# Performance work log

Measured on AMD Instinct MI355X. Metric: run time of the kernel, lower is better.

Reference implementation:

```python
import jax, jax.numpy as jnp
import numpy as np

POOL_K = 8        # predictor_kernel_size
THRESH = 0.05     # predictor_threshold
EPS = 1e-5        # masked_fill value


def _round_ste(x):
    # straight-through round (forward: round)
    return x + jax.lax.stop_gradient(jnp.round(x) - x)


def _quant_act_uint(x, scale, bits):
    # Brevitas Uint8ActPerTensorFloat-style fake quant: unsigned, per-tensor scale
    n = 2.0 ** bits - 1.0
    return jnp.clip(_round_ste(x / scale), 0.0, n) * scale


def _quant_weight_per_oc(w, bits):
    # signed, narrow-range, per-output-channel scaling: s = max|w| / (2^(b-1)-1)
    n = 2.0 ** (bits - 1) - 1.0
    s = jnp.max(jnp.abs(w), axis=(1, 2, 3), keepdims=True) / n
    return jnp.clip(_round_ste(w / s), -n, n) * s


def _conv(x, w):
    return jax.lax.conv_general_dilated(
        x, w, window_strides=(1, 1), padding=((1, 1), (1, 1)),
        dimension_numbers=('NCHW', 'OIHW', 'NCHW'))


def _predictor_mask(x):
    # AvgPool2d(8) (stride=kernel) -> threshold -> nearest upsample back to HxW
    B, C, H, W = x.shape
    pooled = x.reshape(B, C, H // POOL_K, POOL_K, W // POOL_K, POOL_K).mean(axis=(3, 5))
    m = pooled >= THRESH
    m = jnp.repeat(jnp.repeat(m, POOL_K, axis=2), POOL_K, axis=3)  # nearest interp
    return jax.lax.stop_gradient(m)  # mask.detach()


def setup_inputs() -> dict:
    key = jax.random.key(0)
    k1, k2, k3 = jax.random.split(key, 3)
    x = jax.random.normal(k1, (32, 128, 56, 56), jnp.float32)
    w_high = jax.random.normal(k2, (128, 128, 3, 3), jnp.float32) * 0.05
    w_low = jax.random.normal(k3, (128, 128, 3, 3), jnp.float32) * 0.05
    return {
        'x': x,
        'w_high': w_high,
        'w_low': w_low,
        'act_scale_high': jnp.float32(0.02),
        'act_scale_low': jnp.float32(0.04),
    }


def reference(x, w_high, w_low, act_scale_high, act_scale_low):
    mask = _predictor_mask(x)                 # [B,C,H,W] bool
    x_high = jnp.where(mask, x, EPS)          # masked_fill(~mask, 1e-5)
    x_low = jnp.where(mask, EPS, x)           # masked_fill(mask, 1e-5)
    y_high = _conv(_quant_act_uint(x_high, act_scale_high, 8),
                   _quant_weight_per_oc(w_high, 8))
    y_low = _conv(_quant_act_uint(x_low, act_scale_low, 4),
                  _quant_weight_per_oc(w_low, 4))
    return y_high + y_low
```

## Files before the change

### kernel.cpp

```cpp
#include <hip/hip_runtime.h>
#include <hip/hip_bf16.h>
#include <stdint.h>

#define BATCH 32
#define CH 128
#define HH 56
#define WW 56
#define HW 3136
#define M_TOTAL (BATCH*HW)
#define PLANE ((size_t)M_TOTAL * 16)

using int4v   = __attribute__((ext_vector_type(4))) int;
using float4v = __attribute__((ext_vector_type(4))) float;

#define WQB_OFF 0
#define SCB_OFF 294912
#define ZP_OFF  296448
#define AQN_OFF 296704

#define GLD_LDS16(g, l)                                                        \
  __builtin_amdgcn_global_load_lds(                                            \
      (const __attribute__((address_space(1))) void*)(g),                      \
      (__attribute__((address_space(3))) void*)(l), 16, 0, 0)

#define KSTR 484

__global__ __launch_bounds__(256) void prep_kernel(
    const float* __restrict__ x,
    const float* __restrict__ wh, const float* __restrict__ wl,
    const float* __restrict__ p_sh, const float* __restrict__ p_sl,
    char* __restrict__ wqb, float* __restrict__ scb, int* __restrict__ zp,
    char* __restrict__ aqn) {
  __shared__ __align__(16) float smem[16 * KSTR + 128];
  int t = threadIdx.x;

  if (blockIdx.x >= BATCH * 7 * 8) {
    int blk = blockIdx.x - BATCH * 7 * 8;
    int which = blk >> 7, oc = blk & 127;
    if (blk == 0 && t < 64)
      zp[t] = (t < 32) ? 0x80808080 : 0;
    const float* src = (which ? wl : wh) + (size_t)oc * 1152;
    float n = which ? 7.0f : 127.0f;
    float* red = smem;
    int* ired = (int*)(smem + 256);

    float m = 0.0f;
    for (int e = t; e < 1152; e += 256) m = fmaxf(m, fabsf(src[e]));
    red[t] = m;
    __syncthreads();
    for (int s = 128; s > 0; s >>= 1) {
      if (t < s) red[t] = fmaxf(red[t], red[t + s]);
      __syncthreads();
    }
    float scale = red[0] / n;

    int partial = 0;
    for (int e = t; e < 1152; e += 256) {
      int tt = e >> 7, ic = e & 127;
      float q = rintf(src[ic * 9 + tt] / scale);
      q = fminf(fmaxf(q, -n), n);
      int k = (int)q;
      partial += k;
      wqb[((size_t)tt * 128 + oc) * 256 + which * 128 + ic] = (char)k;
    }
    ired[t] = partial;
    __syncthreads();
    for (int s = 128; s > 0; s >>= 1) {
      if (t < s) ired[t] += ired[t + s];
      __syncthreads();
    }
    if (t == 0) {
      float s_act = which ? p_sl[0] : p_sh[0];
      float sc = s_act * scale;
      if (which == 0) {
        scb[oc] = sc;
        scb[256 + oc] = sc * 128.0f * (float)ired[0];
      } else {
        scb[128 + oc] = sc;
      }
    }
    return;
  }

  int bi = blockIdx.x;
  int cg = bi & 7;
  int bb = bi >> 3;
  int b = bb / 7, band = bb - b * 7;
  float* sx = smem;
  float* smk = smem + 16 * KSTR;
  #pragma unroll
  for (int i = 0; i < 7; ++i) {
    int idx = i * 256 + t;
    int k = idx / 112, rem = idx - k * 112;
    int r = rem / 14, w4 = rem - r * 14;
    *(float4v*)(sx + k * KSTR + r * 60 + w4 * 4) =
        *(const float4v*)(x + ((size_t)(b * 128 + cg * 16 + k)) * HW
                            + (band * 8 + r) * 56 + w4 * 4);
  }
  __syncthreads();
  if (t < 112) {
    int k = t / 7, bw = t - (t / 7) * 7;
    float s = 0.0f;
    #pragma unroll
    for (int r = 0; r < 8; ++r)
      #pragma unroll
      for (int j = 0; j < 8; ++j)
        s += sx[k * KSTR + r * 60 + bw * 8 + j];
    smk[t] = (s * (1.0f / 64.0f) >= 0.05f) ? 1.0f : 0.0f;
  }
  __syncthreads();
  float shs = p_sh[0], sls = p_sl[0];
  #pragma unroll
  for (int it = 0; it < 2; ++it) {
    int pos = it * 256 + t;
    if (pos < 448) {
      int r = pos / 56, w = pos - r * 56;
      int h = band * 8 + r;
      size_t gp = (size_t)b * HW + (size_t)h * 56 + w;
      int hw_[4] = {0, 0, 0, 0}, lw_[4] = {0, 0, 0, 0};
      int mcell = w >> 3;
      #pragma unroll
      for (int k = 0; k < 16; ++k) {
        float xv = sx[k * KSTR + r * 60 + w];
        bool mk = smk[k * 7 + mcell] != 0.0f;
        float xh = mk ? xv : 1e-5f;
        int kh = (int)fminf(fmaxf(rintf(xh / shs), 0.0f), 255.0f) - 128;
        float xl = mk ? 1e-5f : xv;
        int kl = (int)fminf(fmaxf(rintf(xl / sls), 0.0f), 15.0f);
        hw_[k >> 2] |= (kh & 0xff) << ((k & 3) * 8);
        lw_[k >> 2] |= (kl & 0xff) << ((k & 3) * 8);
      }
      *(int4v*)(aqn + ((size_t)cg * M_TOTAL + gp) * 16) =
          (int4v){hw_[0], hw_[1], hw_[2], hw_[3]};
      *(int4v*)(aqn + ((size_t)(8 + cg) * M_TOTAL + gp) * 16) =
          (int4v){lw_[0], lw_[1], lw_[2], lw_[3]};
    }
  }
}

__global__ __launch_bounds__(512, 4) void conv_mfma_kernel(
    const char* __restrict__ wqb,
    const char* __restrict__ aqn,
    const char* __restrict__ zp,
    const float* __restrict__ scb,
    float* __restrict__ out) {
  __shared__ __align__(16) char As[2][160 * 64];
  __shared__ __align__(16) char Bs[2][384 * 64];

  int tid = threadIdx.x;
  int lane = tid & 63, wv = tid >> 6;
  int wm = wv >> 2, wn = wv & 3;
  int lr = lane & 15, quad = lane >> 4;
  int bx = blockIdx.x;
  int m0 = (((bx & 7) * 98) + (bx >> 3)) * 128;

  int ng = (wv < 2) ? 2 : 1;
  int sgrp[2] = {wv, wv + 8};
  const char* abase[2];
  const char* zbase[2];
  int avalid[2], ah[2];
  #pragma unroll
  for (int j = 0; j < 2; ++j) {
    int slot = sgrp[j] * 16 + (lane >> 2);
    int q = ((lane & 3) ^ (slot >> 1)) & 3;
    int p = m0 + slot - 16;
    int pv = (p >= 0) && (p < M_TOTAL);
    int pc = pv ? p : 0;
    int bb = pc / HW, rem = pc - bb * HW;
    int hh = rem / 56;
    abase[j] = aqn + (size_t)q * PLANE + (size_t)pc * 16;
    zbase[j] = zp + q * 16;
    avalid[j] = pv;
    ah[j] = hh;
  }
  const char* bbase[3];
  #pragma unroll
  for (int i = 0; i < 3; ++i) {
    int slot = (wv * 3 + i) * 16 + (lane >> 2);
    int qp = (((lane & 3) ^ (slot >> 1)) & 3) * 16;
    int dwi_s = slot >> 7, ocr = slot & 127;
    bbase[i] = wqb + ((size_t)(dwi_s * 128 + ocr)) * 256 + qp;
  }
  int lo_ok[4], hi_ok[4];
  #pragma unroll
  for (int mi = 0; mi < 4; ++mi) {
    int m = m0 + wm * 64 + mi * 16 + lr;
    int w = (m % HW) % 56;
    lo_ok[mi] = (w > 0);
    hi_ok[mi] = (w < 55);
  }

  int4v acch[4][2], accl[4][2];
  #pragma unroll
  for (int mi = 0; mi < 4; ++mi)
    #pragma unroll
    for (int ni = 0; ni < 2; ++ni) {
      acch[mi][ni] = (int4v){0, 0, 0, 0};
      accl[mi][ni] = (int4v){0, 0, 0, 0};
    }

  auto stageA = [&](int s, char* A) {
    int dh3 = s >> 2, icc = s & 3;
    int dh = dh3 - 1;
    #pragma unroll
    for (int j = 0; j < 2; ++j) {
      if (j < ng) {
        int h2 = ah[j] + dh;
        bool ok = avalid[j] && ((unsigned)h2 < (unsigned)HH);
        const char* p = ok ? (abase[j] + dh * (56 * 16) + (size_t)icc * (4 * PLANE))
                           : (zbase[j] + icc * 64);
        GLD_LDS16(p, A + sgrp[j] * 1024);
      }
    }
  };
  auto stageB = [&](int s, char* B) {
    int dh3 = s >> 2, icc = s & 3;
    #pragma unroll
    for (int i = 0; i < 3; ++i)
      GLD_LDS16(bbase[i] + (size_t)dh3 * 98304 + icc * 64,
                B + ((wv * 3 + i) * 16) * 64);
  };

  auto compute = [&](int s, const char* A, const char* B) {
    int icc = s & 3;
    const bool high = (icc < 2);
    const int patv = high ? (int)0x80808080 : 0;
    const int4v pat = (int4v){patv, patv, patv, patv};
    #pragma unroll
    for (int dwi = 0; dwi < 3; ++dwi) {
      int4v af[4], bf[2];
      #pragma unroll
      for (int mi = 0; mi < 4; ++mi) {
        int sA = wm * 64 + mi * 16 + lr + 15 + dwi;
        af[mi] = *(const int4v*)(A + sA * 64 + (((quad ^ (sA >> 1)) & 3) * 16));
        bool ok = (dwi == 1) | (dwi == 0 ? lo_ok[mi] : hi_ok[mi]);
        af[mi] = ok ? af[mi] : pat;
      }
      #pragma unroll
      for (int ni = 0; ni < 2; ++ni) {
        int sB = dwi * 128 + wn * 32 + ni * 16 + lr;
        bf[ni] = *(const int4v*)(B + sB * 64 + (((quad ^ (sB >> 1)) & 3) * 16));
      }
      __builtin_amdgcn_s_setprio(1);
      if (high) {
        #pragma unroll
        for (int mi = 0; mi < 4; ++mi)
          #pragma unroll
          for (int ni = 0; ni < 2; ++ni)
            acch[mi][ni] = __builtin_amdgcn_mfma_i32_16x16x64_i8(
                af[mi], bf[ni], acch[mi][ni], 0, 0, 0);
      } else {
        #pragma unroll
        for (int mi = 0; mi < 4; ++mi)
          #pragma unroll
          for (int ni = 0; ni < 2; ++ni)
            accl[mi][ni] = __builtin_amdgcn_mfma_i32_16x16x64_i8(
                af[mi], bf[ni], accl[mi][ni], 0, 0, 0);
      }
      __builtin_amdgcn_s_setprio(0);
    }
  };

  stageA(0, As[0]);
  stageB(0, Bs[0]);
  __syncthreads();
  #pragma unroll
  for (int s = 0; s < 12; ++s) {
    if (s < 11) {
      stageB(s + 1, Bs[(s + 1) & 1]);
      stageA(s + 1, As[(s + 1) & 1]);
    }
    compute(s, As[s & 1], Bs[s & 1]);
    __syncthreads();
  }

  #pragma unroll
  for (int mi = 0; mi < 4; ++mi) {
    int m = m0 + wm * 64 + mi * 16 + quad * 4;
    int b = m / HW, r = m - b * HW;
    float* obase = out + (size_t)b * (CH * HW) + r;
    #pragma unroll
    for (int ni = 0; ni < 2; ++ni) {
      int oc = wn * 32 + ni * 16 + lr;
      float sch = scb[oc], scl = scb[128 + oc], bs = scb[256 + oc];
      float4v f;
      #pragma unroll
      for (int rg = 0; rg < 4; ++rg)
        f[rg] = sch * (float)acch[mi][ni][rg] + scl * (float)accl[mi][ni][rg] + bs;
      *(float4v*)(obase + (size_t)oc * HW) = f;
    }
  }
}

extern "C" void kernel_launch(void* const* d_in, const int* in_sizes, int n_in,
                              void* d_out, int out_size, void* d_ws, size_t ws_size,
                              hipStream_t stream) {
  const float* x  = (const float*)d_in[0];
  const float* wh = (const float*)d_in[1];
  const float* wl = (const float*)d_in[2];
  const float* sh = (const float*)d_in[3];
  const float* sl = (const float*)d_in[4];
  float* out = (float*)d_out;

  char* ws = (char*)d_ws;
  char* wqb  = ws + WQB_OFF;
  float* scb = (float*)(ws + SCB_OFF);
  int* zp    = (int*)(ws + ZP_OFF);
  char* aqn  = ws + AQN_OFF;

  prep_kernel<<<dim3(BATCH * 7 * 8 + 256), dim3(256), 0, stream>>>(
      x, wh, wl, sh, sl, wqb, scb, zp, aqn);
  conv_mfma_kernel<<<dim3(M_TOTAL / 128), dim3(512), 0, stream>>>(
      wqb, aqn, (const char*)zp, scb, out);
}
```

Baseline: 152.0 us.

## Triple-buffer A tiles and replace syncthreads with vmcnt-gated barriers

Moves LDS to dynamic shared memory with three A buffers and two B buffers. The A tile for stage s+2 is issued after compute(s), and each iteration starts with a waitcnt on outstanding global-to-LDS loads plus a raw s_barrier instead of __syncthreads. The aim is to keep more loads in flight and drop one barrier per stage, so memory latency overlaps with MFMA work. LDS per block grows from 68 KB to 78 KB, which may lower occupancy. The per-wave vmcnt counts depend on how many loads each wave issues, so getting them wrong could cause races.

```diff
diff --git a/kernel.cpp b/kernel.cpp
--- a/kernel.cpp
+++ b/kernel.cpp
@@ -9,6 +9,10 @@
 #define HW 3136
 #define M_TOTAL (BATCH*HW)
 #define PLANE ((size_t)M_TOTAL * 16)
+
+#define A_BUF 10240
+#define B_BUF 24576
+#define LDS_TOTAL (3*A_BUF + 2*B_BUF)
 
 using int4v   = __attribute__((ext_vector_type(4))) int;
 using float4v = __attribute__((ext_vector_type(4))) float;
@@ -144,8 +148,9 @@
     const char* __restrict__ zp,
     const float* __restrict__ scb,
     float* __restrict__ out) {
-  __shared__ __align__(16) char As[2][160 * 64];
-  __shared__ __align__(16) char Bs[2][384 * 64];
+  extern __shared__ __align__(16) char lds[];
+  char* As0 = lds;
+  char* Bs0 = lds + 3 * A_BUF;
 
   int tid = threadIdx.x;
   int lane = tid & 63, wv = tid >> 6;
@@ -261,17 +266,23 @@
     }
   };
 
-  stageA(0, As[0]);
-  stageB(0, Bs[0]);
-  __syncthreads();
+  stageA(0, As0);
+  stageB(0, Bs0);
+  stageA(1, As0 + A_BUF);
   #pragma unroll
   for (int s = 0; s < 12; ++s) {
-    if (s < 11) {
-      stageB(s + 1, Bs[(s + 1) & 1]);
-      stageA(s + 1, As[(s + 1) & 1]);
-    }
-    compute(s, As[s & 1], Bs[s & 1]);
-    __syncthreads();
+    if (s == 11) {
+      asm volatile("s_waitcnt vmcnt(0)" ::: "memory");
+    } else if (wv < 2) {
+      asm volatile("s_waitcnt vmcnt(2)" ::: "memory");
+    } else {
+      asm volatile("s_waitcnt vmcnt(1)" ::: "memory");
+    }
+    __builtin_amdgcn_s_barrier();
+    __builtin_amdgcn_sched_barrier(0);
+    if (s < 11) stageB(s + 1, Bs0 + ((s + 1) & 1) * B_BUF);
+    compute(s, As0 + (s % 3) * A_BUF, Bs0 + (s & 1) * B_BUF);
+    if (s < 10) stageA(s + 2, As0 + ((s + 2) % 3) * A_BUF);
   }
 
   #pragma unroll
@@ -308,8 +319,15 @@
   int* zp    = (int*)(ws + ZP_OFF);
   char* aqn  = ws + AQN_OFF;
 
+  static bool lds_attr_set = false;
+  if (!lds_attr_set) {
+    hipFuncSetAttribute(reinterpret_cast<const void*>(&conv_mfma_kernel),
+                        hipFuncAttributeMaxDynamicSharedMemorySize, LDS_TOTAL);
+    lds_attr_set = true;
+  }
+
   prep_kernel<<<dim3(BATCH * 7 * 8 + 256), dim3(256), 0, stream>>>(
       x, wh, wl, sh, sl, wqb, scb, zp, aqn);
-  conv_mfma_kernel<<<dim3(M_TOTAL / 128), dim3(512), 0, stream>>>(
+  conv_mfma_kernel<<<dim3(M_TOTAL / 128), dim3(512), LDS_TOTAL, stream>>>(
       wqb, aqn, (const char*)zp, scb, out);
 }
```

Result: no change. 149.8 us (-1.4%).
